# Optimization experiments

Measured on AMD Instinct MI355X. Metric: run time of the kernel, lower is better.

## Reference

```python
import jax, jax.numpy as jnp
import numpy as np


def setup_inputs() -> dict:
    key = jax.random.key(0)
    k1, k2, k3, k4, k5 = jax.random.split(key, 5)
    L, B, S, He, Hd = 2, 32, 4096, 1024, 1024
    hidden = jax.random.normal(k1, (L, B, He), dtype=jnp.float32)
    encoder_outputs = jax.random.normal(k2, (B, S, He), dtype=jnp.float32)
    # nn.Linear(2*He, Hd) weight stored transposed here as [2*He, Hd]
    W_attn = jax.random.normal(k3, (2 * He, Hd), dtype=jnp.float32) * (1.0 / np.sqrt(2 * He))
    b_attn = jax.random.normal(k4, (Hd,), dtype=jnp.float32) * 0.01
    # nn.Linear(Hd, 1, bias=False) weight as vector [Hd]
    v_w = jax.random.normal(k5, (Hd,), dtype=jnp.float32) * (1.0 / np.sqrt(Hd))
    return {"hidden": hidden, "encoder_outputs": encoder_outputs,
            "W_attn": W_attn, "b_attn": b_attn, "v_w": v_w}


def reference(hidden, encoder_outputs, W_attn, b_attn, v_w):
    # hidden: [L, B, He]; encoder_outputs: [B, S, He]
    h = hidden[-1]                      # [B, He]
    He = h.shape[-1]
    # concat([h, enc]) @ W == h @ W[:He] + enc @ W[He:]  (avoids materializing concat)
    W_h = W_attn[:He]                   # [He, Hd]
    W_e = W_attn[He:]                   # [He, Hd]
    h_proj = h @ W_h                    # [B, Hd]
    e_proj = jnp.einsum('bse,eh->bsh', encoder_outputs, W_e)  # [B, S, Hd]
    energy = jnp.tanh(h_proj[:, None, :] + e_proj + b_attn)   # [B, S, Hd]
    scores = jnp.einsum('bsh,h->bs', energy, v_w)             # [B, S]
    return jax.nn.softmax(scores, axis=1)
```

## Files before the change

### kernel.cpp

```cpp
#include <hip/hip_runtime.h>
#include <hip/hip_bf16.h>

typedef short s16x8 __attribute__((ext_vector_type(8)));
typedef float f32x16 __attribute__((ext_vector_type(16)));
typedef unsigned short us8 __attribute__((ext_vector_type(8)));

#define HE   1024
#define SEQ  4096
#define NBAT 32
#define BM   64
#define BKG  64
#define NG   16

__device__ __forceinline__ unsigned short f2bf(float f) {
    unsigned u = __builtin_bit_cast(unsigned, f);
    u += 0x7FFFu + ((u >> 16) & 1u);
    return (unsigned short)(u >> 16);
}

__device__ __forceinline__ float tanh_fast(float x) {
    float e = __expf(2.0f * x);
    return 1.0f - 2.0f / (e + 1.0f);
}

#define WG_SYNC() do {                                         \
    asm volatile("s_waitcnt lgkmcnt(0)" ::: "memory");         \
    __builtin_amdgcn_s_barrier();                              \
} while (0)

__global__ void k_hproj(const float* __restrict__ hidden, const float* __restrict__ W,
                        float* __restrict__ cpart) {
    int b = blockIdx.x >> 3, kc = blockIdx.x & 7;
    int h = threadIdx.x;
    const float* hv = hidden + (NBAT + b) * HE;
    int k0 = kc * 128;
    float acc = 0.f;
    for (int j = 0; j < 128; ++j)
        acc = fmaf(hv[k0 + j], W[(k0 + j) * HE + h], acc);
    cpart[(b * 8 + kc) * HE + h] = acc;
}

__global__ void k_cfinal(const float* __restrict__ cpart, const float* __restrict__ b_attn,
                         float* __restrict__ c) {
    int b = blockIdx.x, h = threadIdx.x;
    float s = b_attn[h];
    #pragma unroll
    for (int kc = 0; kc < 8; ++kc) s += cpart[(b * 8 + kc) * HE + h];
    c[b * HE + h] = s;
}

__global__ void k_pack(const float* __restrict__ W, unsigned short* __restrict__ Wp) {
    int gid = blockIdx.x * blockDim.x + threadIdx.x;
    int l = gid & 63, cf = (gid >> 6) & 31, kb2 = gid >> 11;
    int krow = HE + kb2 * 16 + ((l >> 5) * 8);
    int col  = cf * 32 + (l & 31);
    us8 v;
    #pragma unroll
    for (int i = 0; i < 8; ++i) v[i] = f2bf(W[(krow + i) * HE + col]);
    *(us8*)(Wp + (long)gid * 8) = v;
}

__global__ __launch_bounds__(512, 2) void k_main(
    const float* __restrict__ E, const us8* __restrict__ Wp,
    const float* __restrict__ C, const float* __restrict__ VW,
    float* __restrict__ scores)
{
    __shared__ unsigned short Abuf[2][BM * BKG];
    __shared__ float smred[BM][8];

    const int tid  = threadIdx.x;
    const int lane = tid & 63;
    const int wv   = tid >> 6;
    const int m0   = blockIdx.x * BM;
    const int bb   = m0 >> 12;

    const int s_row = tid >> 3;
    const int s_kq  = tid & 7;
    const float* gE = E + (long)(m0 + s_row) * HE + s_kq * 8;
    char* const a_wr0 = (char*)&Abuf[0][0] + s_row * 128 + ((s_kq ^ (s_row & 7)) << 4);
    char* const a_wr1 = (char*)&Abuf[1][0] + s_row * 128 + ((s_kq ^ (s_row & 7)) << 4);

    const int l31 = lane & 31, lh = lane >> 5;
    const int a_sw = l31 & 7;
    const int a_r0 = l31 * 128;
    const int a_r1 = (32 + l31) * 128;

    const char* WpB = (const char*)Wp + ((long)(wv * 4) << 10) + lane * 16;

    f32x16 acc[2][4];
    #pragma unroll
    for (int rf = 0; rf < 2; ++rf)
        #pragma unroll
        for (int cfi = 0; cfi < 4; ++cfi)
            #pragma unroll
            for (int e = 0; e < 16; ++e) acc[rf][cfi][e] = 0.f;

#define LOADB_SET(set, kb2base)                                                  \
    _Pragma("unroll")                                                            \
    for (int s_ = 0; s_ < 2; ++s_)                                               \
        _Pragma("unroll")                                                        \
        for (int cfi = 0; cfi < 4; ++cfi)                                        \
            set[s_ * 4 + cfi] = *(const s16x8*)(WpB +                            \
                (((long)((kb2base) + s_) * 32 + cfi) << 10));

#define AREAD2(d0, d1, Ab, stp) do {                                             \
    const int o_ = ((((stp) * 2 + lh) ^ a_sw) << 4);                             \
    d0 = *(const s16x8*)((Ab) + a_r0 + o_);                                      \
    d1 = *(const s16x8*)((Ab) + a_r1 + o_);                                      \
} while (0)

#define MFMA_STEP(a0_, a1_, bset, si) do {                                       \
    __builtin_amdgcn_s_setprio(1);                                               \
    _Pragma("unroll")                                                            \
    for (int cfi = 0; cfi < 4; ++cfi)                                            \
        acc[0][cfi] = __builtin_amdgcn_mfma_f32_32x32x16_bf16(                   \
            a0_, bset[(si) * 4 + cfi], acc[0][cfi], 0, 0, 0);                    \
    _Pragma("unroll")                                                            \
    for (int cfi = 0; cfi < 4; ++cfi)                                            \
        acc[1][cfi] = __builtin_amdgcn_mfma_f32_32x32x16_bf16(                   \
            a1_, bset[(si) * 4 + cfi], acc[1][cfi], 0, 0, 0);                    \
    __builtin_amdgcn_s_setprio(0);                                               \
} while (0)

#define STAGE_WRITE(ptr) do {                                                    \
    us8 w_;                                                                      \
    w_[0]=f2bf(evA.x); w_[1]=f2bf(evA.y); w_[2]=f2bf(evA.z); w_[3]=f2bf(evA.w);  \
    w_[4]=f2bf(evB.x); w_[5]=f2bf(evB.y); w_[6]=f2bf(evB.z); w_[7]=f2bf(evB.w);  \
    *(us8*)(ptr) = w_;                                                           \
} while (0)

    s16x8 bU[8], bV[8];
    s16x8 x0, x1, y0, y1;
    float4 evA, evB;

    evA = *(const float4*)(gE);
    evB = *(const float4*)(gE + 4);
    LOADB_SET(bU, 0);
    STAGE_WRITE(a_wr0);
    WG_SYNC();

    for (int g = 0; g < NG; ++g) {
        const char* Ab = (const char*)&Abuf[g & 1][0];
        const int kb2 = g * 4;

        LOADB_SET(bV, kb2 + 2);
        if (g + 1 < NG) {
            evA = *(const float4*)(gE + (g + 1) * BKG);
            evB = *(const float4*)(gE + (g + 1) * BKG + 4);
        }

        AREAD2(x0, x1, Ab, 0);
        AREAD2(y0, y1, Ab, 1);
        MFMA_STEP(x0, x1, bU, 0);
        MFMA_STEP(y0, y1, bU, 1);

        {
            const int nb = (g + 1 < NG) ? (kb2 + 4) : kb2;
            LOADB_SET(bU, nb);
        }
        AREAD2(x0, x1, Ab, 2);
        AREAD2(y0, y1, Ab, 3);
        MFMA_STEP(x0, x1, bV, 0);
        MFMA_STEP(y0, y1, bV, 1);

        if (g + 1 < NG) {
            char* awr = (g & 1) ? a_wr0 : a_wr1;
            STAGE_WRITE(awr);
        }
        WG_SYNC();
    }

#undef LOADB_SET
#undef AREAD2
#undef MFMA_STEP
#undef STAGE_WRITE

    float cv[4], vv[4];
    #pragma unroll
    for (int cfi = 0; cfi < 4; ++cfi) {
        int col = (wv * 4 + cfi) * 32 + l31;
        cv[cfi] = C[bb * HE + col];
        vv[cfi] = VW[col];
    }
    #pragma unroll
    for (int rf = 0; rf < 2; ++rf) {
        #pragma unroll
        for (int reg = 0; reg < 16; ++reg) {
            float pS = 0.f;
            #pragma unroll
            for (int cfi = 0; cfi < 4; ++cfi)
                pS += tanh_fast(acc[rf][cfi][reg] + cv[cfi]) * vv[cfi];
            pS += __shfl_xor(pS, 1);
            pS += __shfl_xor(pS, 2);
            pS += __shfl_xor(pS, 4);
            pS += __shfl_xor(pS, 8);
            pS += __shfl_xor(pS, 16);
            if (l31 == 0) {
                int row = rf * 32 + (reg & 3) + 8 * (reg >> 2) + 4 * lh;
                smred[row][wv] = pS;
            }
        }
    }
    __syncthreads();
    if (tid < BM) {
        float s = 0.f;
        #pragma unroll
        for (int ww = 0; ww < 8; ++ww) s += smred[tid][ww];
        scores[m0 + tid] = s;
    }
}

__global__ void k_softmax(const float* __restrict__ scores, float* __restrict__ out) {
    __shared__ float red[16];
    __shared__ float red2[16];
    int b = blockIdx.x, tid = threadIdx.x;
    const float* s = scores + b * SEQ;
    float v[4];
    float mx = -1e30f;
    #pragma unroll
    for (int j = 0; j < 4; ++j) { v[j] = s[tid + j * 1024]; mx = fmaxf(mx, v[j]); }
    #pragma unroll
    for (int off = 32; off; off >>= 1) mx = fmaxf(mx, __shfl_xor(mx, off));
    if ((tid & 63) == 0) red[tid >> 6] = mx;
    __syncthreads();
    mx = red[0];
    #pragma unroll
    for (int i = 1; i < 16; ++i) mx = fmaxf(mx, red[i]);
    float sum = 0.f;
    #pragma unroll
    for (int j = 0; j < 4; ++j) { v[j] = expf(v[j] - mx); sum += v[j]; }
    #pragma unroll
    for (int off = 32; off; off >>= 1) sum += __shfl_xor(sum, off);
    if ((tid & 63) == 0) red2[tid >> 6] = sum;
    __syncthreads();
    sum = 0.f;
    #pragma unroll
    for (int i = 0; i < 16; ++i) sum += red2[i];
    float inv = 1.0f / sum;
    #pragma unroll
    for (int j = 0; j < 4; ++j) out[b * SEQ + tid + j * 1024] = v[j] * inv;
}

extern "C" void kernel_launch(void* const* d_in, const int* in_sizes, int n_in,
                              void* d_out, int out_size, void* d_ws, size_t ws_size,
                              hipStream_t stream)
{
    const float* hidden = (const float*)d_in[0];
    const float* enc    = (const float*)d_in[1];
    const float* W      = (const float*)d_in[2];
    const float* b_attn = (const float*)d_in[3];
    const float* v_w    = (const float*)d_in[4];
    float* out          = (float*)d_out;

    char* ws = (char*)d_ws;
    unsigned short* Wp = (unsigned short*)(ws);
    float* cpart       = (float*)(ws + (2u << 20));
    float* Cc          = (float*)(ws + (3u << 20));
    float* scores      = (float*)(ws + (3u << 20) + (128u << 10));

    k_pack   <<<512, 256,  0, stream>>>(W, Wp);
    k_hproj  <<<256, 1024, 0, stream>>>(hidden, W, cpart);
    k_cfinal <<<32,  1024, 0, stream>>>(cpart, b_attn, Cc);
    k_main   <<<2048, 512, 0, stream>>>(enc, (const us8*)Wp, Cc, v_w, scores);
    k_softmax<<<32,  1024, 0, stream>>>(scores, out);
}
```

Baseline: 452.9 us.

## Stage packed W tiles into LDS via direct global-to-LDS loads

The main GEMM kernel now copies the packed bf16 weight tiles into double-buffered shared memory with global_load_lds, instead of having each wave load its B fragments straight from global memory into registers. The K step is halved to 32 so each buffer holds 64KB of W, and the encoder tile is staged in smaller pieces with a new swizzle. The aim is to cut register pressure and VGPR-bound global latency on B. In exchange it uses about 136KB of LDS per block, which likely breaks the 2-blocks-per-CU target, and it doubles the number of barriers.

```diff
diff --git a/kernel.cpp b/kernel.cpp
--- a/kernel.cpp
+++ b/kernel.cpp
@@ -9,8 +9,8 @@
 #define SEQ  4096
 #define NBAT 32
 #define BM   64
-#define BKG  64
-#define NG   16
+#define BK   32
+#define NC   32
 
 __device__ __forceinline__ unsigned short f2bf(float f) {
     unsigned u = __builtin_bit_cast(unsigned, f);
@@ -23,10 +23,12 @@
     return 1.0f - 2.0f / (e + 1.0f);
 }
 
-#define WG_SYNC() do {                                         \
-    asm volatile("s_waitcnt lgkmcnt(0)" ::: "memory");         \
-    __builtin_amdgcn_s_barrier();                              \
-} while (0)
+__device__ __forceinline__ void gload_lds16(const void* g, void* l) {
+    __builtin_amdgcn_global_load_lds(
+        (const __attribute__((address_space(1))) unsigned int*)g,
+        (__attribute__((address_space(3))) unsigned int*)l,
+        16, 0, 0);
+}
 
 __global__ void k_hproj(const float* __restrict__ hidden, const float* __restrict__ W,
                         float* __restrict__ cpart) {
@@ -61,11 +63,12 @@
 }
 
 __global__ __launch_bounds__(512, 2) void k_main(
-    const float* __restrict__ E, const us8* __restrict__ Wp,
+    const float* __restrict__ E, const unsigned short* __restrict__ Wp,
     const float* __restrict__ C, const float* __restrict__ VW,
     float* __restrict__ scores)
 {
-    __shared__ unsigned short Abuf[2][BM * BKG];
+    __shared__ unsigned short Bbuf[2][32768];
+    __shared__ unsigned short Ebuf[2][2048];
     __shared__ float smred[BM][8];
 
     const int tid  = threadIdx.x;
@@ -73,19 +76,18 @@
     const int wv   = tid >> 6;
     const int m0   = blockIdx.x * BM;
     const int bb   = m0 >> 12;
+    const int l31  = lane & 31, lh = lane >> 5;
 
     const int s_row = tid >> 3;
     const int s_kq  = tid & 7;
-    const float* gE = E + (long)(m0 + s_row) * HE + s_kq * 8;
-    char* const a_wr0 = (char*)&Abuf[0][0] + s_row * 128 + ((s_kq ^ (s_row & 7)) << 4);
-    char* const a_wr1 = (char*)&Abuf[1][0] + s_row * 128 + ((s_kq ^ (s_row & 7)) << 4);
-
-    const int l31 = lane & 31, lh = lane >> 5;
-    const int a_sw = l31 & 7;
-    const int a_r0 = l31 * 128;
-    const int a_r1 = (32 + l31) * 128;
-
-    const char* WpB = (const char*)Wp + ((long)(wv * 4) << 10) + lane * 16;
+    const float* gE = E + (long)(m0 + s_row) * HE + s_kq * 4;
+    const int e_wo = s_row * 64 + (((s_kq >> 1) ^ (s_row & 3)) << 4) + (s_kq & 1) * 8;
+
+    const int a_o0 = l31 * 64;
+    const int a_o1 = (32 + l31) * 64;
+    const int a_sw = l31 & 3;
+
+    const char* WpB = (const char*)Wp;
 
     f32x16 acc[2][4];
     #pragma unroll
@@ -95,85 +97,78 @@
             #pragma unroll
             for (int e = 0; e < 16; ++e) acc[rf][cfi][e] = 0.f;
 
-#define LOADB_SET(set, kb2base)                                                  \
-    _Pragma("unroll")                                                            \
-    for (int s_ = 0; s_ < 2; ++s_)                                               \
-        _Pragma("unroll")                                                        \
-        for (int cfi = 0; cfi < 4; ++cfi)                                        \
-            set[s_ * 4 + cfi] = *(const s16x8*)(WpB +                            \
-                (((long)((kb2base) + s_) * 32 + cfi) << 10));
-
-#define AREAD2(d0, d1, Ab, stp) do {                                             \
+#define STAGE_B(pb, g1) do {                                                     \
+    const char* src_ = WpB + (((long)(g1) * 64 + wv * 8) << 10) + (lane << 4);   \
+    char* dst_ = (char*)&Bbuf[pb][0] + ((wv * 8) << 10);                         \
+    _Pragma("unroll")                                                            \
+    for (int r_ = 0; r_ < 8; ++r_)                                               \
+        gload_lds16(src_ + (r_ << 10), dst_ + (r_ << 10));                       \
+} while (0)
+
+#define E_WRITE(pb) do {                                                         \
+    ushort4 w_;                                                                  \
+    w_.x = f2bf(evq.x); w_.y = f2bf(evq.y);                                      \
+    w_.z = f2bf(evq.z); w_.w = f2bf(evq.w);                                      \
+    *(ushort4*)((char*)&Ebuf[pb][0] + e_wo) = w_;                                \
+} while (0)
+
+#define AREAD(d0, d1, pb, stp) do {                                              \
     const int o_ = ((((stp) * 2 + lh) ^ a_sw) << 4);                             \
-    d0 = *(const s16x8*)((Ab) + a_r0 + o_);                                      \
-    d1 = *(const s16x8*)((Ab) + a_r1 + o_);                                      \
-} while (0)
-
-#define MFMA_STEP(a0_, a1_, bset, si) do {                                       \
+    d0 = *(const s16x8*)((const char*)&Ebuf[pb][0] + a_o0 + o_);                 \
+    d1 = *(const s16x8*)((const char*)&Ebuf[pb][0] + a_o1 + o_);                 \
+} while (0)
+
+#define BREAD(bv, pb, stp)                                                       \
+    _Pragma("unroll")                                                            \
+    for (int cfi = 0; cfi < 4; ++cfi)                                            \
+        bv[cfi] = *(const s16x8*)((const char*)&Bbuf[pb][0] +                    \
+            (((stp) * 32 + wv * 4 + cfi) << 10) + (lane << 4));
+
+#define MFMA8(a0_, a1_, bv) do {                                                 \
     __builtin_amdgcn_s_setprio(1);                                               \
     _Pragma("unroll")                                                            \
     for (int cfi = 0; cfi < 4; ++cfi)                                            \
         acc[0][cfi] = __builtin_amdgcn_mfma_f32_32x32x16_bf16(                   \
-            a0_, bset[(si) * 4 + cfi], acc[0][cfi], 0, 0, 0);                    \
+            a0_, bv[cfi], acc[0][cfi], 0, 0, 0);                                 \
     _Pragma("unroll")                                                            \
     for (int cfi = 0; cfi < 4; ++cfi)                                            \
         acc[1][cfi] = __builtin_amdgcn_mfma_f32_32x32x16_bf16(                   \
-            a1_, bset[(si) * 4 + cfi], acc[1][cfi], 0, 0, 0);                    \
+            a1_, bv[cfi], acc[1][cfi], 0, 0, 0);                                 \
     __builtin_amdgcn_s_setprio(0);                                               \
 } while (0)
 
-#define STAGE_WRITE(ptr) do {                                                    \
-    us8 w_;                                                                      \
-    w_[0]=f2bf(evA.x); w_[1]=f2bf(evA.y); w_[2]=f2bf(evA.z); w_[3]=f2bf(evA.w);  \
-    w_[4]=f2bf(evB.x); w_[5]=f2bf(evB.y); w_[6]=f2bf(evB.z); w_[7]=f2bf(evB.w);  \
-    *(us8*)(ptr) = w_;                                                           \
-} while (0)
-
-    s16x8 bU[8], bV[8];
-    s16x8 x0, x1, y0, y1;
-    float4 evA, evB;
-
-    evA = *(const float4*)(gE);
-    evB = *(const float4*)(gE + 4);
-    LOADB_SET(bU, 0);
-    STAGE_WRITE(a_wr0);
-    WG_SYNC();
-
-    for (int g = 0; g < NG; ++g) {
-        const char* Ab = (const char*)&Abuf[g & 1][0];
-        const int kb2 = g * 4;
-
-        LOADB_SET(bV, kb2 + 2);
-        if (g + 1 < NG) {
-            evA = *(const float4*)(gE + (g + 1) * BKG);
-            evB = *(const float4*)(gE + (g + 1) * BKG + 4);
+    float4 evq;
+
+    evq = *(const float4*)(gE);
+    STAGE_B(0, 0);
+    E_WRITE(0);
+    __syncthreads();
+
+    for (int g = 0; g < NC; ++g) {
+        const int p = g & 1;
+        s16x8 x0, x1, y0, y1, bs0[4], bs1[4];
+
+        if (g + 1 < NC) {
+            evq = *(const float4*)(gE + (g + 1) * BK);
+            STAGE_B(p ^ 1, g + 1);
         }
 
-        AREAD2(x0, x1, Ab, 0);
-        AREAD2(y0, y1, Ab, 1);
-        MFMA_STEP(x0, x1, bU, 0);
-        MFMA_STEP(y0, y1, bU, 1);
-
-        {
-            const int nb = (g + 1 < NG) ? (kb2 + 4) : kb2;
-            LOADB_SET(bU, nb);
-        }
-        AREAD2(x0, x1, Ab, 2);
-        AREAD2(y0, y1, Ab, 3);
-        MFMA_STEP(x0, x1, bV, 0);
-        MFMA_STEP(y0, y1, bV, 1);
-
-        if (g + 1 < NG) {
-            char* awr = (g & 1) ? a_wr0 : a_wr1;
-            STAGE_WRITE(awr);
-        }
-        WG_SYNC();
-    }
-
-#undef LOADB_SET
-#undef AREAD2
-#undef MFMA_STEP
-#undef STAGE_WRITE
+        AREAD(x0, x1, p, 0);
+        BREAD(bs0, p, 0);
+        AREAD(y0, y1, p, 1);
+        BREAD(bs1, p, 1);
+        MFMA8(x0, x1, bs0);
+        MFMA8(y0, y1, bs1);
+
+        if (g + 1 < NC) E_WRITE(p ^ 1);
+        __syncthreads();
+    }
+
+#undef STAGE_B
+#undef E_WRITE
+#undef AREAD
+#undef BREAD
+#undef MFMA8
 
     float cv[4], vv[4];
     #pragma unroll
@@ -261,6 +256,6 @@
     k_pack   <<<512, 256,  0, stream>>>(W, Wp);
     k_hproj  <<<256, 1024, 0, stream>>>(hidden, W, cpart);
     k_cfinal <<<32,  1024, 0, stream>>>(cpart, b_attn, Cc);
-    k_main   <<<2048, 512, 0, stream>>>(enc, (const us8*)Wp, Cc, v_w, scores);
+    k_main   <<<2048, 512, 0, stream>>>(enc, Wp, Cc, v_w, scores);
     k_softmax<<<32,  1024, 0, stream>>>(scores, out);
 }
```

Result: slower. 575.3 us (+27.0%).

## Use 16-wave blocks with 2 column tiles per wave and deeper A prefetch

Applied to the files above, without the earlier changes.

The main GEMM kernel now uses 1024-thread blocks (16 waves), and each wave owns 2 column tiles instead of 4. The A tile is staged in 128-wide K chunks, with E loads prefetched two groups ahead. B fragments are double-buffered per MFMA step, and the whole loop is fully unrolled. The goal is more waves in flight to hide memory latency and fewer per-wave registers. The cost is that each A fragment read from LDS is reused across only 2 MFMAs per row tile, which doubles LDS traffic relative to compute, and launch_bounds(1024,4) may cause register spills.

```diff
diff --git a/kernel.cpp b/kernel.cpp
--- a/kernel.cpp
+++ b/kernel.cpp
@@ -5,12 +5,13 @@
 typedef float f32x16 __attribute__((ext_vector_type(16)));
 typedef unsigned short us8 __attribute__((ext_vector_type(8)));
 
-#define HE   1024
-#define SEQ  4096
-#define NBAT 32
-#define BM   64
-#define BKG  64
-#define NG   16
+#define HE    1024
+#define SEQ   4096
+#define NBAT  32
+#define BM    64
+#define KSUB  128
+#define NGRP  8
+#define NSTEP 8
 
 __device__ __forceinline__ unsigned short f2bf(float f) {
     unsigned u = __builtin_bit_cast(unsigned, f);
@@ -51,8 +52,8 @@
 
 __global__ void k_pack(const float* __restrict__ W, unsigned short* __restrict__ Wp) {
     int gid = blockIdx.x * blockDim.x + threadIdx.x;
-    int l = gid & 63, cf = (gid >> 6) & 31, kb2 = gid >> 11;
-    int krow = HE + kb2 * 16 + ((l >> 5) * 8);
+    int l = gid & 63, cf = (gid >> 6) & 31, kst = gid >> 11;
+    int krow = HE + kst * 16 + ((l >> 5) * 8);
     int col  = cf * 32 + (l & 31);
     us8 v;
     #pragma unroll
@@ -60,127 +61,126 @@
     *(us8*)(Wp + (long)gid * 8) = v;
 }
 
-__global__ __launch_bounds__(512, 2) void k_main(
-    const float* __restrict__ E, const us8* __restrict__ Wp,
+__global__ __launch_bounds__(1024, 4) void k_main(
+    const float* __restrict__ E, const unsigned short* __restrict__ Wp,
     const float* __restrict__ C, const float* __restrict__ VW,
     float* __restrict__ scores)
 {
-    __shared__ unsigned short Abuf[2][BM * BKG];
-    __shared__ float smred[BM][8];
+    __shared__ unsigned short Asub[2][BM * KSUB];
+    __shared__ float smred[BM][16];
 
     const int tid  = threadIdx.x;
     const int lane = tid & 63;
     const int wv   = tid >> 6;
     const int m0   = blockIdx.x * BM;
     const int bb   = m0 >> 12;
-
-    const int s_row = tid >> 3;
-    const int s_kq  = tid & 7;
-    const float* gE = E + (long)(m0 + s_row) * HE + s_kq * 8;
-    char* const a_wr0 = (char*)&Abuf[0][0] + s_row * 128 + ((s_kq ^ (s_row & 7)) << 4);
-    char* const a_wr1 = (char*)&Abuf[1][0] + s_row * 128 + ((s_kq ^ (s_row & 7)) << 4);
-
-    const int l31 = lane & 31, lh = lane >> 5;
+    const int l31  = lane & 31, lh = lane >> 5;
+
+    const int s_row = tid >> 4;
+    const int s_kc  = tid & 15;
+    const float* gEs = E + (long)(m0 + s_row) * HE + s_kc * 8;
+    const int e_wo = s_row * 256 + ((s_kc ^ (s_row & 7)) << 4);
+
     const int a_sw = l31 & 7;
-    const int a_r0 = l31 * 128;
-    const int a_r1 = (32 + l31) * 128;
-
-    const char* WpB = (const char*)Wp + ((long)(wv * 4) << 10) + lane * 16;
-
-    f32x16 acc[2][4];
+    const int a_r0 = l31 * 256;
+    const int a_r1 = (32 + l31) * 256;
+
+    const char* WpB = (const char*)Wp + (((long)(wv * 2)) << 10) + (lane << 4);
+
+    f32x16 acc[2][2];
     #pragma unroll
     for (int rf = 0; rf < 2; ++rf)
         #pragma unroll
-        for (int cfi = 0; cfi < 4; ++cfi)
+        for (int cf = 0; cf < 2; ++cf)
             #pragma unroll
-            for (int e = 0; e < 16; ++e) acc[rf][cfi][e] = 0.f;
-
-#define LOADB_SET(set, kb2base)                                                  \
-    _Pragma("unroll")                                                            \
-    for (int s_ = 0; s_ < 2; ++s_)                                               \
-        _Pragma("unroll")                                                        \
-        for (int cfi = 0; cfi < 4; ++cfi)                                        \
-            set[s_ * 4 + cfi] = *(const s16x8*)(WpB +                            \
-                (((long)((kb2base) + s_) * 32 + cfi) << 10));
-
-#define AREAD2(d0, d1, Ab, stp) do {                                             \
-    const int o_ = ((((stp) * 2 + lh) ^ a_sw) << 4);                             \
-    d0 = *(const s16x8*)((Ab) + a_r0 + o_);                                      \
-    d1 = *(const s16x8*)((Ab) + a_r1 + o_);                                      \
-} while (0)
-
-#define MFMA_STEP(a0_, a1_, bset, si) do {                                       \
+            for (int e = 0; e < 16; ++e) acc[rf][cf][e] = 0.f;
+
+#define LOADB(dst, kst) do {                                                     \
+    dst[0] = *(const s16x8*)(WpB + (((long)(kst) * 32 + 0) << 10));              \
+    dst[1] = *(const s16x8*)(WpB + (((long)(kst) * 32 + 1) << 10));              \
+} while (0)
+
+#define AREAD(buf, s) do {                                                       \
+    const char* Ab_ = (const char*)&Asub[buf][0];                                \
+    const int o_ = (((2 * (s) + lh)) ^ a_sw) << 4;                               \
+    a0 = *(const s16x8*)(Ab_ + a_r0 + o_);                                       \
+    a1 = *(const s16x8*)(Ab_ + a_r1 + o_);                                       \
+} while (0)
+
+#define MFMA4(bv) do {                                                           \
     __builtin_amdgcn_s_setprio(1);                                               \
-    _Pragma("unroll")                                                            \
-    for (int cfi = 0; cfi < 4; ++cfi)                                            \
-        acc[0][cfi] = __builtin_amdgcn_mfma_f32_32x32x16_bf16(                   \
-            a0_, bset[(si) * 4 + cfi], acc[0][cfi], 0, 0, 0);                    \
-    _Pragma("unroll")                                                            \
-    for (int cfi = 0; cfi < 4; ++cfi)                                            \
-        acc[1][cfi] = __builtin_amdgcn_mfma_f32_32x32x16_bf16(                   \
-            a1_, bset[(si) * 4 + cfi], acc[1][cfi], 0, 0, 0);                    \
+    acc[0][0] = __builtin_amdgcn_mfma_f32_32x32x16_bf16(a0, bv[0], acc[0][0], 0, 0, 0); \
+    acc[0][1] = __builtin_amdgcn_mfma_f32_32x32x16_bf16(a0, bv[1], acc[0][1], 0, 0, 0); \
+    acc[1][0] = __builtin_amdgcn_mfma_f32_32x32x16_bf16(a1, bv[0], acc[1][0], 0, 0, 0); \
+    acc[1][1] = __builtin_amdgcn_mfma_f32_32x32x16_bf16(a1, bv[1], acc[1][1], 0, 0, 0); \
     __builtin_amdgcn_s_setprio(0);                                               \
 } while (0)
 
-#define STAGE_WRITE(ptr) do {                                                    \
+#define EV_LOAD(vA, vB, g2) do {                                                 \
+    vA = *(const float4*)(gEs + (g2) * KSUB);                                    \
+    vB = *(const float4*)(gEs + (g2) * KSUB + 4);                                \
+} while (0)
+
+#define EV_WRITE(vA, vB, buf) do {                                               \
     us8 w_;                                                                      \
-    w_[0]=f2bf(evA.x); w_[1]=f2bf(evA.y); w_[2]=f2bf(evA.z); w_[3]=f2bf(evA.w);  \
-    w_[4]=f2bf(evB.x); w_[5]=f2bf(evB.y); w_[6]=f2bf(evB.z); w_[7]=f2bf(evB.w);  \
-    *(us8*)(ptr) = w_;                                                           \
-} while (0)
-
-    s16x8 bU[8], bV[8];
-    s16x8 x0, x1, y0, y1;
-    float4 evA, evB;
-
-    evA = *(const float4*)(gE);
-    evB = *(const float4*)(gE + 4);
-    LOADB_SET(bU, 0);
-    STAGE_WRITE(a_wr0);
+    w_[0]=f2bf(vA.x); w_[1]=f2bf(vA.y); w_[2]=f2bf(vA.z); w_[3]=f2bf(vA.w);      \
+    w_[4]=f2bf(vB.x); w_[5]=f2bf(vB.y); w_[6]=f2bf(vB.z); w_[7]=f2bf(vB.w);      \
+    *(us8*)((char*)&Asub[buf][0] + e_wo) = w_;                                   \
+} while (0)
+
+    s16x8 bE[2], bO[2], a0, a1;
+    float4 eA0, eA1, eB0, eB1;
+
+    EV_LOAD(eA0, eA1, 0);
+    EV_LOAD(eB0, eB1, 1);
+    LOADB(bE, 0);
+    EV_WRITE(eA0, eA1, 0);
     WG_SYNC();
 
-    for (int g = 0; g < NG; ++g) {
-        const char* Ab = (const char*)&Abuf[g & 1][0];
-        const int kb2 = g * 4;
-
-        LOADB_SET(bV, kb2 + 2);
-        if (g + 1 < NG) {
-            evA = *(const float4*)(gE + (g + 1) * BKG);
-            evB = *(const float4*)(gE + (g + 1) * BKG + 4);
+    #pragma unroll
+    for (int g = 0; g < NGRP; ++g) {
+        const int buf = g & 1;
+
+        #pragma unroll
+        for (int s = 0; s < NSTEP; ++s) {
+            int nk = g * NSTEP + s + 1;
+            if (nk > 63) nk = 63;
+            if ((s & 1) == 0) {
+                LOADB(bO, nk);
+                AREAD(buf, s);
+                MFMA4(bE);
+            } else {
+                LOADB(bE, nk);
+                AREAD(buf, s);
+                MFMA4(bO);
+            }
         }
 
-        AREAD2(x0, x1, Ab, 0);
-        AREAD2(y0, y1, Ab, 1);
-        MFMA_STEP(x0, x1, bU, 0);
-        MFMA_STEP(y0, y1, bU, 1);
-
-        {
-            const int nb = (g + 1 < NG) ? (kb2 + 4) : kb2;
-            LOADB_SET(bU, nb);
+        if (g < NGRP - 1) {
+            if ((g & 1) == 0) {
+                if (g < NGRP - 2) EV_LOAD(eA0, eA1, g + 2);
+                EV_WRITE(eB0, eB1, 1);
+            } else {
+                if (g < NGRP - 2) EV_LOAD(eB0, eB1, g + 2);
+                EV_WRITE(eA0, eA1, 0);
+            }
+            __builtin_amdgcn_sched_barrier(0);
+            WG_SYNC();
         }
-        AREAD2(x0, x1, Ab, 2);
-        AREAD2(y0, y1, Ab, 3);
-        MFMA_STEP(x0, x1, bV, 0);
-        MFMA_STEP(y0, y1, bV, 1);
-
-        if (g + 1 < NG) {
-            char* awr = (g & 1) ? a_wr0 : a_wr1;
-            STAGE_WRITE(awr);
-        }
-        WG_SYNC();
-    }
-
-#undef LOADB_SET
-#undef AREAD2
-#undef MFMA_STEP
-#undef STAGE_WRITE
-
-    float cv[4], vv[4];
-    #pragma unroll
-    for (int cfi = 0; cfi < 4; ++cfi) {
-        int col = (wv * 4 + cfi) * 32 + l31;
-        cv[cfi] = C[bb * HE + col];
-        vv[cfi] = VW[col];
+    }
+
+#undef LOADB
+#undef AREAD
+#undef MFMA4
+#undef EV_LOAD
+#undef EV_WRITE
+
+    float cv[2], vv[2];
+    #pragma unroll
+    for (int cf = 0; cf < 2; ++cf) {
+        int col = (wv * 2 + cf) * 32 + l31;
+        cv[cf] = C[bb * HE + col];
+        vv[cf] = VW[col];
     }
     #pragma unroll
     for (int rf = 0; rf < 2; ++rf) {
@@ -188,8 +188,8 @@
         for (int reg = 0; reg < 16; ++reg) {
             float pS = 0.f;
             #pragma unroll
-            for (int cfi = 0; cfi < 4; ++cfi)
-                pS += tanh_fast(acc[rf][cfi][reg] + cv[cfi]) * vv[cfi];
+            for (int cf = 0; cf < 2; ++cf)
+                pS += tanh_fast(acc[rf][cf][reg] + cv[cf]) * vv[cf];
             pS += __shfl_xor(pS, 1);
             pS += __shfl_xor(pS, 2);
             pS += __shfl_xor(pS, 4);
@@ -205,7 +205,7 @@
     if (tid < BM) {
         float s = 0.f;
         #pragma unroll
-        for (int ww = 0; ww < 8; ++ww) s += smred[tid][ww];
+        for (int ww = 0; ww < 16; ++ww) s += smred[tid][ww];
         scores[m0 + tid] = s;
     }
 }
@@ -261,6 +261,6 @@
     k_pack   <<<512, 256,  0, stream>>>(W, Wp);
     k_hproj  <<<256, 1024, 0, stream>>>(hidden, W, cpart);
     k_cfinal <<<32,  1024, 0, stream>>>(cpart, b_attn, Cc);
-    k_main   <<<2048, 512, 0, stream>>>(enc, (const us8*)Wp, Cc, v_w, scores);
+    k_main   <<<2048, 1024, 0, stream>>>(enc, Wp, Cc, v_w, scores);
     k_softmax<<<32,  1024, 0, stream>>>(scores, out);
 }
```

After: 417.1 us. 7.9% less time.
